# Performance work log

Measured on AMD Instinct MI355X. Metric: run time of the kernel, lower is better.

The kernel has to match this reference:

```python
import jax, jax.numpy as jnp
import numpy as np
from jax import lax

EPS = 1e-5
NUM_CLASSES = 133


def conv2d(x, w, stride, pad, b=None):
    # x: [N,C,H,W], w: [O,I,kh,kw]
    out = lax.conv_general_dilated(x, w, (stride, stride), ((pad, pad), (pad, pad)),
                                   dimension_numbers=('NCHW', 'OIHW', 'NCHW'))
    if b is not None:
        out = out + b[None, :, None, None]
    return out


def cbn(x, y, embed_w, C):
    # ConditionalBatchNorm2d in training mode: batch stats (biased var), affine from embedding
    mean = x.mean(axis=(0, 2, 3), keepdims=True)
    var = x.var(axis=(0, 2, 3), keepdims=True)
    xn = (x - mean) * lax.rsqrt(var + EPS)
    gb = embed_w[y]                      # [O, 2C]
    gamma, beta = gb[:, :C], gb[:, C:]
    return gamma[:, :, None, None] * xn + beta[:, :, None, None]


def lrelu(x):
    return jnp.where(x >= 0, x, 0.2 * x)


def clstm_layer(x_seq, w, b, hidden_dim):
    # x_seq: [T, B, Cin, 16, 16] -> (all h: [T,B,hid,16,16], last h: [B,hid,16,16])
    B = x_seq.shape[1]
    h0 = jnp.zeros((B, hidden_dim, 16, 16), x_seq.dtype)

    def step(carry, x):
        h, c = carry
        cc = conv2d(jnp.concatenate([x, h], axis=1), w, 1, 2, b)  # k=5, pad=2
        i, f, o, g = jnp.split(cc, 4, axis=1)
        c = jax.nn.sigmoid(f) * c + jax.nn.sigmoid(i) * jnp.tanh(g)
        h = jax.nn.sigmoid(o) * jnp.tanh(c)
        return (h, c), h

    (h, _), hs = lax.scan(step, (h0, h0), x_seq)
    return hs, h


def setup_inputs() -> dict:
    key = jax.random.key(0)
    ks = jax.random.split(key, 24)
    O, C_in, H = 8, 512, 254
    B, T = 4, 2
    d = {}
    d['h'] = jax.random.normal(ks[0], (O, C_in, H, H), jnp.float32)
    d['objs'] = jax.random.randint(ks[1], (O,), 0, NUM_CLASSES)
    d['obj_to_img'] = jnp.repeat(jnp.arange(B), T)  # sorted, equal-sized groups

    def w(k, shape):
        fan_in = shape[1] * shape[2] * shape[3]
        return jax.random.normal(k, shape, jnp.float32) / np.sqrt(fan_in)

    def embed(k, C):
        g = 1.0 + 0.02 * jax.random.normal(k, (NUM_CLASSES, C), jnp.float32)
        return jnp.concatenate([g, jnp.zeros((NUM_CLASSES, C), jnp.float32)], axis=1)

    d['c1_w'] = w(ks[2], (32, 512, 1, 1))
    d['c2_w'] = w(ks[3], (64, 32, 4, 4))
    d['c3_w'] = w(ks[4], (128, 64, 4, 4))
    d['c4_w'] = w(ks[5], (256, 128, 4, 4))
    d['c5_w'] = w(ks[6], (512, 256, 4, 4))
    d['e1'] = embed(ks[7], 32)
    d['e2'] = embed(ks[8], 64)
    d['e3'] = embed(ks[9], 128)
    d['e4'] = embed(ks[10], 256)
    d['e5'] = embed(ks[11], 512)
    # ConvLSTM layers: hidden [128, 64, 64], kernel 5x5, input_dim 512
    d['lw0'] = w(ks[12], (4 * 128, 512 + 128, 5, 5))
    d['lb0'] = jnp.zeros((4 * 128,), jnp.float32)
    d['lw1'] = w(ks[13], (4 * 64, 128 + 64, 5, 5))
    d['lb1'] = jnp.zeros((4 * 64,), jnp.float32)
    d['lw2'] = w(ks[14], (4 * 64, 64 + 64, 5, 5))
    d['lb2'] = jnp.zeros((4 * 64,), jnp.float32)
    return d


def reference(objs, obj_to_img, h, c1_w, c2_w, c3_w, c4_w, c5_w,
              e1, e2, e3, e4, e5, lw0, lb0, lw1, lb1, lw2, lb2):
    x = lrelu(cbn(conv2d(h, c1_w, 1, 1), objs, e1, 32))    # [O,32,256,256]
    x = lrelu(cbn(conv2d(x, c2_w, 2, 1), objs, e2, 64))    # [O,64,128,128]
    x = lrelu(cbn(conv2d(x, c3_w, 2, 1), objs, e3, 128))   # [O,128,64,64]
    x = cbn(conv2d(x, c4_w, 2, 1), objs, e4, 256)          # no activation after bn4 (as in source)
    x = cbn(conv2d(x, c5_w, 2, 1), objs, e5, 512)          # [O,512,16,16], no activation after bn5

    # Group ragged per-image object sequences. The torch loop groups consecutive
    # equal obj_to_img ids; with equal group sizes this is a static reshape.
    o2i = np.asarray(obj_to_img)
    B = int(o2i.max()) + 1
    O = x.shape[0]
    T = O // B
    assert B * T == O, 'reference assumes equal-sized, sorted object groups'
    seq = x.reshape(B, T, 512, 16, 16).transpose(1, 0, 2, 3, 4)  # [T,B,512,16,16]

    hs, _ = clstm_layer(seq, lw0, lb0, 128)
    hs, _ = clstm_layer(hs, lw1, lb1, 64)
    _, h_last = clstm_layer(hs, lw2, lb2, 64)
    return h_last  # [B,64,16,16]
```

## Files before the change

kernel.cpp:

```cpp
#include <hip/hip_runtime.h>
#include <math.h>

#define LEAK 0.2f

typedef __attribute__((ext_vector_type(8))) short bf16x8;
typedef __attribute__((ext_vector_type(4))) float f32x4;

__device__ __forceinline__ unsigned short f2bf(float f) {
  unsigned u = __float_as_uint(f);
  u += 0x7FFFu + ((u >> 16) & 1u);
  return (unsigned short)(u >> 16);
}
__device__ __forceinline__ unsigned pack2(float a, float b) {
  return (unsigned)f2bf(a) | ((unsigned)f2bf(b) << 16);
}

#define MFMA16(a, b, c) __builtin_amdgcn_mfma_f32_16x16x32_bf16(a, b, c, 0, 0, 0)

__device__ __forceinline__ void wprep_std(
    const float* __restrict__ w, unsigned short* __restrict__ dst,
    int O, int C, int TAPS, int i)
{
  int o = i / (C * TAPS);
  int r = i - o * C * TAPS;
  int c = r / TAPS, tap = r - c * TAPS;
  dst[((size_t)tap * O + o) * C + c] = f2bf(w[i]);
}

__global__ __launch_bounds__(256) void wprepAll_kernel(
    const float* c1w, const float* c2w, const float* c3w, const float* c4w,
    const float* c5w, const float* lw0, const float* lw1, const float* lw2,
    unsigned short* wb1, unsigned short* wb2, unsigned short* wb3,
    unsigned short* wb4, unsigned short* wb5, unsigned short* wbf0,
    unsigned short* wbf1, unsigned short* wbf2)
{
  int i = blockIdx.x * 256 + threadIdx.x;
  if (i < 16384) {
    int o = i >> 9, c = i & 511;
    wb1[(((c >> 5) * 32) + o) * 32 + (c & 31)] = f2bf(c1w[i]);
    return;
  }
  i -= 16384;
  if (i < 32768)   { wprep_std(c2w, wb2, 64, 32, 16, i);    return; }
  i -= 32768;
  if (i < 131072)  { wprep_std(c3w, wb3, 128, 64, 16, i);   return; }
  i -= 131072;
  if (i < 524288)  { wprep_std(c4w, wb4, 256, 128, 16, i);  return; }
  i -= 524288;
  if (i < 2097152) { wprep_std(c5w, wb5, 512, 256, 16, i);  return; }
  i -= 2097152;
  if (i < 8192000) { wprep_std(lw0, wbf0, 512, 640, 25, i); return; }
  i -= 8192000;
  if (i < 1228800) { wprep_std(lw1, wbf1, 256, 192, 25, i); return; }
  i -= 1228800;
  if (i < 819200)  { wprep_std(lw2, wbf2, 256, 128, 25, i); return; }
}

__global__ __launch_bounds__(256) void conv1M_kernel(
    const float* __restrict__ h, const unsigned short* __restrict__ wbc,
    float* __restrict__ xT, float* __restrict__ part1)
{
  __shared__ __align__(16) unsigned short inT[2][256 * 40];
  __shared__ float red1[4][4][2][4][2];

  const int n = blockIdx.y, r = blockIdx.x;
  const int px0 = r * 256;
  const int tid = threadIdx.x, lane = tid & 63, wid = tid >> 6;
  const int ln15 = lane & 15, kg = lane >> 4;
  const bool rint = (r >= 1 && r <= 254);

  f32x4 acc[2][4];
#pragma unroll
  for (int m = 0; m < 2; ++m)
#pragma unroll
    for (int f = 0; f < 4; ++f) acc[m][f] = (f32x4){0.f, 0.f, 0.f, 0.f};

#define STAGE1(KC, BUF)                                                          \
  {                                                                              \
    _Pragma("unroll")                                                            \
    for (int k = 0; k < 4; ++k) {                                                \
      const int ch = 2 * (k * 4 + wid);                                          \
      const int c0 = 4 * lane;                                                   \
      const float* p0 = h + ((size_t)(n * 512 + (KC) * 32 + ch)) * 64516         \
                          + (size_t)(r - 1) * 254 + (c0 - 1);                    \
      const float* p1 = p0 + 64516;                                              \
      float v0[4], v1[4];                                                        \
      _Pragma("unroll")                                                          \
      for (int j = 0; j < 4; ++j) {                                              \
        const int c = c0 + j;                                                    \
        const bool ok = rint && (c >= 1) && (c <= 254);                          \
        v0[j] = ok ? p0[j] : 0.f;                                                \
        v1[j] = ok ? p1[j] : 0.f;                                                \
      }                                                                          \
      const int chs = ch ^ ((lane & 3) << 3);                                    \
      _Pragma("unroll")                                                          \
      for (int j = 0; j < 4; ++j)                                                \
        *(unsigned*)&inT[BUF][(c0 + j) * 40 + chs] = pack2(v0[j], v1[j]);        \
    }                                                                            \
  }

  STAGE1(0, 0);
  __syncthreads();
  for (int kc = 0; kc < 16; ++kc) {
    if (kc < 15) STAGE1(kc + 1, (kc + 1) & 1);
    const bf16x8 a0 = *(const bf16x8*)(wbc + ((size_t)(kc * 32 + ln15)) * 32 + kg * 8);
    const bf16x8 a1 = *(const bf16x8*)(wbc + ((size_t)(kc * 32 + 16 + ln15)) * 32 + kg * 8);
    const int cur = kc & 1;
#pragma unroll
    for (int f = 0; f < 4; ++f) {
      const int pxr = wid * 64 + f * 16 + ln15;
      const int chs = (kg * 8) ^ (((pxr >> 2) & 3) << 3);
      const bf16x8 b = *(const bf16x8*)&inT[cur][pxr * 40 + chs];
      acc[0][f] = MFMA16(a0, b, acc[0][f]);
      acc[1][f] = MFMA16(a1, b, acc[1][f]);
    }
    __syncthreads();
  }
#undef STAGE1

#pragma unroll
  for (int mf = 0; mf < 2; ++mf) {
#pragma unroll
    for (int f = 0; f < 4; ++f) {
      const int px = px0 + wid * 64 + f * 16 + ln15;
      const int o = mf * 16 + kg * 4;
      *(f32x4*)(xT + ((size_t)n * 65536 + px) * 32 + o) = acc[mf][f];
    }
  }

#pragma unroll
  for (int mf = 0; mf < 2; ++mf) {
#pragma unroll
    for (int j = 0; j < 4; ++j) {
      float s = 0.f, q = 0.f;
#pragma unroll
      for (int f = 0; f < 4; ++f) { float v = acc[mf][f][j]; s += v; q += v * v; }
#pragma unroll
      for (int mk = 1; mk < 16; mk <<= 1) {
        s += __shfl_xor(s, mk);
        q += __shfl_xor(q, mk);
      }
      if (ln15 == 0) { red1[wid][kg][mf][j][0] = s; red1[wid][kg][mf][j][1] = q; }
    }
  }
  __syncthreads();
  if (tid < 32) {
    const int mf = tid >> 4, kgi = (tid >> 2) & 3, j = tid & 3;
    float s = red1[0][kgi][mf][j][0] + red1[1][kgi][mf][j][0]
            + red1[2][kgi][mf][j][0] + red1[3][kgi][mf][j][0];
    float q = red1[0][kgi][mf][j][1] + red1[1][kgi][mf][j][1]
            + red1[2][kgi][mf][j][1] + red1[3][kgi][mf][j][1];
    atomicAdd(&part1[tid], s);
    atomicAdd(&part1[32 + tid], q);
  }
}

__global__ __launch_bounds__(256) void cbn1T_kernel(
    const float* __restrict__ xT, const float* __restrict__ part1, float invN,
    const float* __restrict__ e1, const int* __restrict__ objs,
    unsigned short* __restrict__ T2)
{
  __shared__ float st[32][4];
  const int n = blockIdx.y;
  if (threadIdx.x < 32) {
    int y = objs[n];
    float s = part1[threadIdx.x], q = part1[32 + threadIdx.x];
    float mean = s * invN;
    st[threadIdx.x][0] = mean;
    st[threadIdx.x][1] = rsqrtf(q * invN - mean * mean + 1e-5f);
    st[threadIdx.x][2] = e1[(size_t)y * 64 + threadIdx.x];
    st[threadIdx.x][3] = e1[(size_t)y * 64 + 32 + threadIdx.x];
  }
  __syncthreads();
  const int pix = blockIdx.x * 256 + threadIdx.x;
  const int r = pix >> 8, c = pix & 255;
  const float* src = xT + ((size_t)n * 65536 + pix) * 32;
  unsigned short* dst = T2 + ((size_t)n * 66564 + (size_t)(r + 1) * 258 + (c + 1)) * 32;
  unsigned outw[16];
#pragma unroll
  for (int q = 0; q < 8; ++q) {
    float4 t = ((const float4*)src)[q];
    float v[4] = {t.x, t.y, t.z, t.w};
#pragma unroll
    for (int j = 0; j < 4; ++j) {
      int ch = q * 4 + j;
      float z = (v[j] - st[ch][0]) * st[ch][1] * st[ch][2] + st[ch][3];
      v[j] = z >= 0.f ? z : LEAK * z;
    }
    outw[2 * q]     = pack2(v[0], v[1]);
    outw[2 * q + 1] = pack2(v[2], v[3]);
  }
  uint4* d4 = (uint4*)dst;
#pragma unroll
  for (int q = 0; q < 4; ++q)
    d4[q] = make_uint4(outw[4*q], outw[4*q+1], outw[4*q+2], outw[4*q+3]);
}

template <int C, int O, int H, int WM>
__global__ __launch_bounds__(256) void conv4T_kernel(
    const unsigned short* __restrict__ Tin, const unsigned short* __restrict__ wb,
    float* __restrict__ raw, float* __restrict__ part)
{
  constexpr int HIN2 = 2 * H + 2;
  constexpr int KC = C / 32;
  constexpr int WN4 = 4 / WM;
  constexpr int NT = WM;
  constexpr int LOGH = (H == 128 ? 7 : (H == 64 ? 6 : (H == 32 ? 5 : 4)));
  __shared__ float red[4][4][2][4][2];
  const int o0 = blockIdx.x * (WM * 32);
  const int strip = blockIdx.y;
  const int n = blockIdx.z;
  const int tid = threadIdx.x, lane = tid & 63, wid = tid >> 6;
  const int wm = wid / WN4, wn = wid % WN4;
  const int ln15 = lane & 15, kg = lane >> 4;
  const unsigned short* inb = Tin + (size_t)n * (HIN2 * HIN2) * C;

  f32x4 acc[2][NT];
#pragma unroll
  for (int m = 0; m < 2; ++m)
#pragma unroll
    for (int nt = 0; nt < NT; ++nt) acc[m][nt] = (f32x4){0.f, 0.f, 0.f, 0.f};

  int r_[NT], c_[NT];
#pragma unroll
  for (int nt = 0; nt < NT; ++nt) {
    const int gp = strip * 64 + (wn * NT + nt) * 16;
    r_[nt] = gp >> LOGH;
    c_[nt] = (gp & (H - 1)) + ln15;
  }

  for (int kc = 0; kc < KC; ++kc) {
    const int cb = kc * 32 + kg * 8;
#pragma unroll
    for (int tap = 0; tap < 16; ++tap) {
      const int ky = tap >> 2, kx = tap & 3;
      const unsigned short* ap = wb + ((size_t)tap * O + o0 + wm * 32 + ln15) * C + cb;
      bf16x8 a0 = *(const bf16x8*)ap;
      bf16x8 a1 = *(const bf16x8*)(ap + (size_t)16 * C);
#pragma unroll
      for (int nt = 0; nt < NT; ++nt) {
        bf16x8 b = *(const bf16x8*)(inb + (size_t)((2 * r_[nt] + ky) * HIN2 + 2 * c_[nt] + kx) * C + cb);
        acc[0][nt] = MFMA16(a0, b, acc[0][nt]);
        acc[1][nt] = MFMA16(a1, b, acc[1][nt]);
      }
    }
  }

#pragma unroll
  for (int mf = 0; mf < 2; ++mf) {
    const int o = o0 + wm * 32 + mf * 16 + kg * 4;
#pragma unroll
    for (int nt = 0; nt < NT; ++nt) {
      const int gp = strip * 64 + (wn * NT + nt) * 16 + ln15;
      *(f32x4*)(raw + ((size_t)n * (H * H) + gp) * O + o) = acc[mf][nt];
    }
  }

#pragma unroll
  for (int mf = 0; mf < 2; ++mf) {
#pragma unroll
    for (int j = 0; j < 4; ++j) {
      float s = 0.f, q = 0.f;
#pragma unroll
      for (int nt = 0; nt < NT; ++nt) { float v = acc[mf][nt][j]; s += v; q += v * v; }
#pragma unroll
      for (int mk = 1; mk < 16; mk <<= 1) {
        s += __shfl_xor(s, mk);
        q += __shfl_xor(q, mk);
      }
      if (ln15 == 0) { red[wid][kg][mf][j][0] = s; red[wid][kg][mf][j][1] = q; }
    }
  }
  __syncthreads();
  if (tid < WM * 32) {
    const int wmi = tid >> 5, mf = (tid >> 4) & 1, kgi = (tid >> 2) & 3, j = tid & 3;
    float s = 0.f, q = 0.f;
#pragma unroll
    for (int w = 0; w < WN4; ++w) {
      s += red[wmi * WN4 + w][kgi][mf][j][0];
      q += red[wmi * WN4 + w][kgi][mf][j][1];
    }
    atomicAdd(&part[o0 + tid], s);
    atomicAdd(&part[O + o0 + tid], q);
  }
}

template <int C, int H, int P2, int CSO, bool LRELU, bool LMAP>
__global__ __launch_bounds__(256) void cbnT_kernel(
    const float* __restrict__ raw, const float* __restrict__ part, float invN,
    const float* __restrict__ embed, const int* __restrict__ objs,
    unsigned short* __restrict__ Tout)
{
  constexpr int W2 = H + 2 * P2;
  constexpr int LOGH = (H == 128 ? 7 : (H == 64 ? 6 : (H == 32 ? 5 : 4)));
  const int n = blockIdx.y;
  const int y = objs[n];
  const int pix = blockIdx.x * 64 + (threadIdx.x >> 2);
  const int r = pix >> LOGH, c = pix & (H - 1);
  const float* src = raw + ((size_t)n * (H * H) + pix) * C;
  const size_t nb = LMAP ? (size_t)((n & 1) * 4 + (n >> 1)) * (W2 * W2) * CSO
                         : (size_t)n * (W2 * W2) * CSO;
  unsigned short* dst = Tout + nb + ((size_t)(r + P2) * W2 + c + P2) * CSO;
  const float* gam = embed + (size_t)y * 2 * C;
  const float* bet = gam + C;
  for (int cs = (threadIdx.x & 3); cs < C / 8; cs += 4) {
    float4 ps0 = ((const float4*)part)[cs * 2],       ps1 = ((const float4*)part)[cs * 2 + 1];
    float4 pq0 = ((const float4*)(part + C))[cs * 2], pq1 = ((const float4*)(part + C))[cs * 2 + 1];
    float4 g0 = ((const float4*)gam)[cs * 2], g1 = ((const float4*)gam)[cs * 2 + 1];
    float4 b0 = ((const float4*)bet)[cs * 2], b1 = ((const float4*)bet)[cs * 2 + 1];
    float4 v0 = ((const float4*)src)[cs * 2], v1 = ((const float4*)src)[cs * 2 + 1];
    float sv[8] = {ps0.x, ps0.y, ps0.z, ps0.w, ps1.x, ps1.y, ps1.z, ps1.w};
    float qv[8] = {pq0.x, pq0.y, pq0.z, pq0.w, pq1.x, pq1.y, pq1.z, pq1.w};
    float gv[8] = {g0.x, g0.y, g0.z, g0.w, g1.x, g1.y, g1.z, g1.w};
    float bv[8] = {b0.x, b0.y, b0.z, b0.w, b1.x, b1.y, b1.z, b1.w};
    float vv[8] = {v0.x, v0.y, v0.z, v0.w, v1.x, v1.y, v1.z, v1.w};
    float o_[8];
#pragma unroll
    for (int k = 0; k < 8; ++k) {
      float m = sv[k] * invN;
      float rs = rsqrtf(qv[k] * invN - m * m + 1e-5f);
      float z = (vv[k] - m) * rs * gv[k] + bv[k];
      o_[k] = (LRELU && z < 0.f) ? LEAK * z : z;
    }
    ((uint4*)dst)[cs] = make_uint4(pack2(o_[0], o_[1]), pack2(o_[2], o_[3]),
                                   pack2(o_[4], o_[5]), pack2(o_[6], o_[7]));
  }
}

template <int O, int CS, int WM, int WN>
__global__ __launch_bounds__(256) void conv5L_kernel(
    const unsigned short* __restrict__ Lin, const unsigned short* __restrict__ wbf,
    float* __restrict__ pp, int kbeg, int slot0, size_t lin_tstr, size_t pp_tstr)
{
  constexpr int FN = 16 / WN;
  const int o0 = blockIdx.x * (WM * 32);
  const int b = blockIdx.y & 3, t = blockIdx.y >> 2;
  const int ks = blockIdx.z;
  const int tid = threadIdx.x, lane = tid & 63, wid = tid >> 6;
  const int wm = wid / WN, wn = wid % WN;
  const int ln15 = lane & 15, kg = lane >> 4;
  const unsigned short* inb = Lin + (size_t)t * lin_tstr + (size_t)b * 400 * CS;
  float* ppb = pp + (size_t)t * pp_tstr + ((size_t)(slot0 + ks) * 4 + b) * (256 * O);

  f32x4 acc[2][FN];
#pragma unroll
  for (int m = 0; m < 2; ++m)
#pragma unroll
    for (int nt = 0; nt < FN; ++nt) acc[m][nt] = (f32x4){0.f, 0.f, 0.f, 0.f};

  const int cb = (kbeg + ks) * 32 + kg * 8;
  for (int tap = 0; tap < 25; ++tap) {
    const int ty = tap / 5, tx = tap - 5 * ty;
    const unsigned short* ap = wbf + ((size_t)tap * O + o0 + wm * 32 + ln15) * CS + cb;
    bf16x8 a0 = *(const bf16x8*)ap;
    bf16x8 a1 = *(const bf16x8*)(ap + (size_t)16 * CS);
#pragma unroll
    for (int nt = 0; nt < FN; ++nt) {
      const int p = (wn * FN + nt) * 16 + ln15;
      const int prow = p >> 4, pcol = p & 15;
      bf16x8 bfv = *(const bf16x8*)(inb + (size_t)((prow + ty) * 20 + pcol + tx) * CS + cb);
      acc[0][nt] = MFMA16(a0, bfv, acc[0][nt]);
      acc[1][nt] = MFMA16(a1, bfv, acc[1][nt]);
    }
  }

#pragma unroll
  for (int mf = 0; mf < 2; ++mf) {
    const int o = o0 + wm * 32 + mf * 16 + kg * 4;
#pragma unroll
    for (int nt = 0; nt < FN; ++nt) {
      const int pix = (wn * FN + nt) * 16 + ln15;
      *(f32x4*)(ppb + (size_t)pix * O + o) = acc[mf][nt];
    }
  }
}

template <int Hc, int CS, int CX, int CSN>
__global__ __launch_bounds__(256) void lstm_pointT_kernel(
    const float* __restrict__ pp, int KS, const float* __restrict__ bias,
    float* __restrict__ cT, unsigned short* __restrict__ own,
    unsigned short* __restrict__ nxt, float* __restrict__ fout)
{
  constexpr int C4 = Hc / 4;
  constexpr int O = 4 * Hc;
  constexpr int LOGC4 = (C4 == 32 ? 5 : 4);
  const int i = blockIdx.x * 256 + threadIdx.x;
  const int c4 = i & (C4 - 1);
  const int pix = (i >> LOGC4) & 255;
  const int b = i >> (LOGC4 + 8);

  float g[4][4];
#pragma unroll
  for (int gt = 0; gt < 4; ++gt)
#pragma unroll
    for (int j = 0; j < 4; ++j) g[gt][j] = 0.f;

  for (int ks = 0; ks < KS; ++ks) {
    const float* base = pp + (((size_t)(ks * 4 + b)) * 256 + pix) * O + c4 * 4;
#pragma unroll
    for (int gt = 0; gt < 4; ++gt) {
      float4 v = *(const float4*)(base + gt * Hc);
      g[gt][0] += v.x; g[gt][1] += v.y; g[gt][2] += v.z; g[gt][3] += v.w;
    }
  }
#pragma unroll
  for (int gt = 0; gt < 4; ++gt) {
    float4 bv = *(const float4*)(bias + gt * Hc + c4 * 4);
    g[gt][0] += bv.x; g[gt][1] += bv.y; g[gt][2] += bv.z; g[gt][3] += bv.w;
  }

  float* cp = cT + ((size_t)b * 256 + pix) * Hc + c4 * 4;
  float4 cold = *(const float4*)cp;
  float co[4] = {cold.x, cold.y, cold.z, cold.w};
  float hn[4];
#pragma unroll
  for (int j = 0; j < 4; ++j) {
    float si = 1.f / (1.f + expf(-g[0][j]));
    float sf = 1.f / (1.f + expf(-g[1][j]));
    float so = 1.f / (1.f + expf(-g[2][j]));
    float cn = sf * co[j] + si * tanhf(g[3][j]);
    co[j] = cn;
    hn[j] = so * tanhf(cn);
  }
  *(float4*)cp = make_float4(co[0], co[1], co[2], co[3]);

  const int prow = pix >> 4, pcol = pix & 15;
  const int ppix = (prow + 2) * 20 + pcol + 2;
  uint2 hb = make_uint2(pack2(hn[0], hn[1]), pack2(hn[2], hn[3]));
  if (own) *(uint2*)(own + ((size_t)b * 400 + ppix) * CS + CX + c4 * 4) = hb;
  if (nxt) *(uint2*)(nxt + ((size_t)b * 400 + ppix) * CSN + c4 * 4) = hb;
  if (fout) {
#pragma unroll
    for (int j = 0; j < 4; ++j)
      fout[((size_t)b * Hc + c4 * 4 + j) * 256 + pix] = hn[j];
  }
}

extern "C" void kernel_launch(void* const* d_in, const int* in_sizes, int n_in,
                              void* d_out, int out_size, void* d_ws, size_t ws_size,
                              hipStream_t stream)
{
  const float* h    = (const float*)d_in[0];
  const int*   objs = (const int*)  d_in[1];
  const float* c1w  = (const float*)d_in[3];
  const float* c2w  = (const float*)d_in[4];
  const float* c3w  = (const float*)d_in[5];
  const float* c4w  = (const float*)d_in[6];
  const float* c5w  = (const float*)d_in[7];
  const float* e1   = (const float*)d_in[8];
  const float* e2   = (const float*)d_in[9];
  const float* e3   = (const float*)d_in[10];
  const float* e4   = (const float*)d_in[11];
  const float* e5   = (const float*)d_in[12];
  const float* lw0  = (const float*)d_in[13];
  const float* lb0  = (const float*)d_in[14];
  const float* lw1  = (const float*)d_in[15];
  const float* lb1  = (const float*)d_in[16];
  const float* lw2  = (const float*)d_in[17];
  const float* lb2  = (const float*)d_in[18];

  char* p = (char*)d_ws;
  auto alloc = [&](size_t bytes) { char* r = p; p += (bytes + 255) & ~(size_t)255; return r; };
  float* x1T  = (float*)alloc((size_t)8 * 65536 * 32 * 4);
  float* raw2 = (float*)alloc((size_t)8 * 16384 * 64 * 4);
  float* raw3 = (float*)alloc((size_t)8 * 4096 * 128 * 4);
  float* raw4 = (float*)alloc((size_t)8 * 1024 * 256 * 4);
  float* raw5 = (float*)alloc((size_t)8 * 256 * 512 * 4);
  float* pp   = (float*)alloc((size_t)2 * 20 * 4 * 256 * 512 * 4);
  unsigned short* wb1  = (unsigned short*)alloc((size_t)32 * 512 * 2);
  unsigned short* wb2  = (unsigned short*)alloc((size_t)16 * 64 * 32 * 2);
  unsigned short* wb3  = (unsigned short*)alloc((size_t)16 * 128 * 64 * 2);
  unsigned short* wb4  = (unsigned short*)alloc((size_t)16 * 256 * 128 * 2);
  unsigned short* wb5  = (unsigned short*)alloc((size_t)16 * 512 * 256 * 2);
  unsigned short* wbf0 = (unsigned short*)alloc((size_t)25 * 512 * 640 * 2);
  unsigned short* wbf1 = (unsigned short*)alloc((size_t)25 * 256 * 192 * 2);
  unsigned short* wbf2 = (unsigned short*)alloc((size_t)25 * 256 * 128 * 2);
  char* zbase = p;
  unsigned short* T2 = (unsigned short*)alloc((size_t)8 * 66564 * 32 * 2);
  unsigned short* T3 = (unsigned short*)alloc((size_t)8 * 16900 * 64 * 2);
  unsigned short* T4 = (unsigned short*)alloc((size_t)8 * 4356 * 128 * 2);
  unsigned short* T5 = (unsigned short*)alloc((size_t)8 * 1156 * 256 * 2);
  unsigned short* L0in = (unsigned short*)alloc((size_t)2 * 4 * 400 * 640 * 2);
  unsigned short* L1in = (unsigned short*)alloc((size_t)2 * 4 * 400 * 192 * 2);
  unsigned short* L2in = (unsigned short*)alloc((size_t)2 * 4 * 400 * 128 * 2);
  float* cT0 = (float*)alloc((size_t)4 * 256 * 128 * 4);
  float* cT1 = (float*)alloc((size_t)4 * 256 * 64 * 4);
  float* cT2 = (float*)alloc((size_t)4 * 256 * 64 * 4);
  float* part1 = (float*)alloc(2 * 32 * 4);
  float* part2 = (float*)alloc(2 * 64 * 4);
  float* part3 = (float*)alloc(2 * 128 * 4);
  float* part4 = (float*)alloc(2 * 256 * 4);
  float* part5 = (float*)alloc(2 * 512 * 4);
  size_t zsize = (size_t)(p - zbase);

  hipMemsetAsync(zbase, 0, zsize, stream);
  wprepAll_kernel<<<(13041664 + 255) / 256, 256, 0, stream>>>(
      c1w, c2w, c3w, c4w, c5w, lw0, lw1, lw2,
      wb1, wb2, wb3, wb4, wb5, wbf0, wbf1, wbf2);

  conv1M_kernel<<<dim3(256, 8), 256, 0, stream>>>(h, wb1, x1T, part1);
  cbn1T_kernel<<<dim3(256, 8), 256, 0, stream>>>(x1T, part1, 1.f / (float)(8 * 65536), e1, objs, T2);

  conv4T_kernel<32, 64, 128, 2><<<dim3(1, 256, 8), 256, 0, stream>>>(T2, wb2, raw2, part2);
  cbnT_kernel<64, 128, 1, 64, true, false><<<dim3(256, 8), 256, 0, stream>>>(
      raw2, part2, 1.f / (float)(8 * 16384), e2, objs, T3);

  conv4T_kernel<64, 128, 64, 2><<<dim3(2, 64, 8), 256, 0, stream>>>(T3, wb3, raw3, part3);
  cbnT_kernel<128, 64, 1, 128, true, false><<<dim3(64, 8), 256, 0, stream>>>(
      raw3, part3, 1.f / (float)(8 * 4096), e3, objs, T4);

  conv4T_kernel<128, 256, 32, 1><<<dim3(8, 16, 8), 256, 0, stream>>>(T4, wb4, raw4, part4);
  cbnT_kernel<256, 32, 1, 256, false, false><<<dim3(16, 8), 256, 0, stream>>>(
      raw4, part4, 1.f / (float)(8 * 1024), e4, objs, T5);

  conv4T_kernel<256, 512, 16, 1><<<dim3(16, 4, 8), 256, 0, stream>>>(T5, wb5, raw5, part5);
  cbnT_kernel<512, 16, 2, 640, false, true><<<dim3(4, 8), 256, 0, stream>>>(
      raw5, part5, 1.f / (float)(8 * 256), e5, objs, L0in);

  {
    const size_t LINT = (size_t)4 * 400 * 640;
    const size_t PPT  = (size_t)20 * 4 * 256 * 512;
    conv5L_kernel<512, 640, 2, 2><<<dim3(8, 8, 16), 256, 0, stream>>>(
        L0in, wbf0, pp, 0, 0, LINT, PPT);
    lstm_pointT_kernel<128, 640, 512, 192><<<128, 256, 0, stream>>>(
        pp, 16, lb0, cT0, L0in + LINT, L1in, nullptr);
    conv5L_kernel<512, 640, 2, 2><<<dim3(8, 4, 4), 256, 0, stream>>>(
        L0in + LINT, wbf0, pp + PPT, 16, 16, 0, 0);
    lstm_pointT_kernel<128, 640, 512, 192><<<128, 256, 0, stream>>>(
        pp + PPT, 20, lb0, cT0, nullptr, L1in + (size_t)4 * 400 * 192, nullptr);
  }

  {
    const size_t LINT = (size_t)4 * 400 * 192;
    const size_t PPT  = (size_t)6 * 4 * 256 * 256;
    conv5L_kernel<256, 192, 1, 4><<<dim3(8, 8, 4), 256, 0, stream>>>(
        L1in, wbf1, pp, 0, 0, LINT, PPT);
    lstm_pointT_kernel<64, 192, 128, 128><<<64, 256, 0, stream>>>(
        pp, 4, lb1, cT1, L1in + LINT, L2in, nullptr);
    conv5L_kernel<256, 192, 1, 4><<<dim3(8, 4, 2), 256, 0, stream>>>(
        L1in + LINT, wbf1, pp + PPT, 4, 4, 0, 0);
    lstm_pointT_kernel<64, 192, 128, 128><<<64, 256, 0, stream>>>(
        pp + PPT, 6, lb1, cT1, nullptr, L2in + (size_t)4 * 400 * 128, nullptr);
  }

  {
    const size_t LINT = (size_t)4 * 400 * 128;
    const size_t PPT  = (size_t)4 * 4 * 256 * 256;
    conv5L_kernel<256, 128, 1, 4><<<dim3(8, 8, 2), 256, 0, stream>>>(
        L2in, wbf2, pp, 0, 0, LINT, PPT);
    lstm_pointT_kernel<64, 128, 64, 1><<<64, 256, 0, stream>>>(
        pp, 2, lb2, cT2, L2in + LINT, nullptr, nullptr);
    conv5L_kernel<256, 128, 1, 4><<<dim3(8, 4, 2), 256, 0, stream>>>(
        L2in + LINT, wbf2, pp + PPT, 2, 2, 0, 0);
    lstm_pointT_kernel<64, 128, 64, 1><<<64, 256, 0, stream>>>(
        pp + PPT, 4, lb2, cT2, nullptr, nullptr, (float*)d_out);
  }
}
```

Baseline: 1.095 ms.

## Transpose weight prep through LDS and widen conv1 tile to two rows

Weight conversion is restructured so each block loads contiguous (o,c,tap) data into shared memory and writes each tap plane with coalesced stores, replacing scattered per-element writes. The first 1x1 conv now processes 512 pixels per block with more accumulators per wave. It drops double-buffered staging in favor of a simple load-sync-compute loop. This trades load/compute overlap for larger tiles and fewer blocks.

Result: faster. 1.041 ms (-4.9%).

```diff
diff --git a/kernel.cpp b/kernel.cpp
--- a/kernel.cpp
+++ b/kernel.cpp
@@ -17,112 +17,110 @@
 
 #define MFMA16(a, b, c) __builtin_amdgcn_mfma_f32_16x16x32_bf16(a, b, c, 0, 0, 0)
 
-__device__ __forceinline__ void wprep_std(
-    const float* __restrict__ w, unsigned short* __restrict__ dst,
-    int O, int C, int TAPS, int i)
-{
-  int o = i / (C * TAPS);
-  int r = i - o * C * TAPS;
-  int c = r / TAPS, tap = r - c * TAPS;
-  dst[((size_t)tap * O + o) * C + c] = f2bf(w[i]);
-}
-
-__global__ __launch_bounds__(256) void wprepAll_kernel(
+__global__ __launch_bounds__(256) void wprepT_kernel(
     const float* c1w, const float* c2w, const float* c3w, const float* c4w,
     const float* c5w, const float* lw0, const float* lw1, const float* lw2,
     unsigned short* wb1, unsigned short* wb2, unsigned short* wb3,
     unsigned short* wb4, unsigned short* wb5, unsigned short* wbf0,
     unsigned short* wbf1, unsigned short* wbf2)
 {
-  int i = blockIdx.x * 256 + threadIdx.x;
-  if (i < 16384) {
+  __shared__ float lds[256 * 26];
+  const int tid = threadIdx.x;
+  int b = blockIdx.x;
+
+  const float* src;
+  unsigned short* dst;
+  int T, OC, base;
+  if (b < 8)         { src = c2w; dst = wb2;  T = 16; OC = 2048;   base = b * 256; }
+  else if (b < 40)   { src = c3w; dst = wb3;  T = 16; OC = 8192;   base = (b - 8) * 256; }
+  else if (b < 168)  { src = c4w; dst = wb4;  T = 16; OC = 32768;  base = (b - 40) * 256; }
+  else if (b < 680)  { src = c5w; dst = wb5;  T = 16; OC = 131072; base = (b - 168) * 256; }
+  else if (b < 872)  { src = lw1; dst = wbf1; T = 25; OC = 49152;  base = (b - 680) * 256; }
+  else if (b < 1000) { src = lw2; dst = wbf2; T = 25; OC = 32768;  base = (b - 872) * 256; }
+  else if (b < 2280) { src = lw0; dst = wbf0; T = 25; OC = 327680; base = (b - 1000) * 256; }
+  else {
+    int i = (b - 2280) * 256 + tid;
     int o = i >> 9, c = i & 511;
     wb1[(((c >> 5) * 32) + o) * 32 + (c & 31)] = f2bf(c1w[i]);
     return;
   }
-  i -= 16384;
-  if (i < 32768)   { wprep_std(c2w, wb2, 64, 32, 16, i);    return; }
-  i -= 32768;
-  if (i < 131072)  { wprep_std(c3w, wb3, 128, 64, 16, i);   return; }
-  i -= 131072;
-  if (i < 524288)  { wprep_std(c4w, wb4, 256, 128, 16, i);  return; }
-  i -= 524288;
-  if (i < 2097152) { wprep_std(c5w, wb5, 512, 256, 16, i);  return; }
-  i -= 2097152;
-  if (i < 8192000) { wprep_std(lw0, wbf0, 512, 640, 25, i); return; }
-  i -= 8192000;
-  if (i < 1228800) { wprep_std(lw1, wbf1, 256, 192, 25, i); return; }
-  i -= 1228800;
-  if (i < 819200)  { wprep_std(lw2, wbf2, 256, 128, 25, i); return; }
+
+  const float* sp = src + (size_t)base * T;
+  for (int e = tid; e < 256 * T; e += 256) {
+    int oc = e / T, tap = e - oc * T;
+    lds[oc * 26 + tap] = sp[e];
+  }
+  __syncthreads();
+  for (int tap = 0; tap < T; ++tap)
+    dst[(size_t)tap * OC + base + tid] = f2bf(lds[tid * 26 + tap]);
 }
 
 __global__ __launch_bounds__(256) void conv1M_kernel(
     const float* __restrict__ h, const unsigned short* __restrict__ wbc,
     float* __restrict__ xT, float* __restrict__ part1)
 {
-  __shared__ __align__(16) unsigned short inT[2][256 * 40];
+  __shared__ __align__(16) unsigned short inT[512 * 40];
   __shared__ float red1[4][4][2][4][2];
 
-  const int n = blockIdx.y, r = blockIdx.x;
-  const int px0 = r * 256;
+  const int n = blockIdx.y;
+  const int px0 = blockIdx.x * 512;
   const int tid = threadIdx.x, lane = tid & 63, wid = tid >> 6;
   const int ln15 = lane & 15, kg = lane >> 4;
-  const bool rint = (r >= 1 && r <= 254);
-
-  f32x4 acc[2][4];
+
+  f32x4 acc[2][8];
 #pragma unroll
   for (int m = 0; m < 2; ++m)
 #pragma unroll
-    for (int f = 0; f < 4; ++f) acc[m][f] = (f32x4){0.f, 0.f, 0.f, 0.f};
-
-#define STAGE1(KC, BUF)                                                          \
-  {                                                                              \
-    _Pragma("unroll")                                                            \
-    for (int k = 0; k < 4; ++k) {                                                \
-      const int ch = 2 * (k * 4 + wid);                                          \
-      const int c0 = 4 * lane;                                                   \
-      const float* p0 = h + ((size_t)(n * 512 + (KC) * 32 + ch)) * 64516         \
-                          + (size_t)(r - 1) * 254 + (c0 - 1);                    \
-      const float* p1 = p0 + 64516;                                              \
-      float v0[4], v1[4];                                                        \
-      _Pragma("unroll")                                                          \
-      for (int j = 0; j < 4; ++j) {                                              \
-        const int c = c0 + j;                                                    \
-        const bool ok = rint && (c >= 1) && (c <= 254);                          \
-        v0[j] = ok ? p0[j] : 0.f;                                                \
-        v1[j] = ok ? p1[j] : 0.f;                                                \
-      }                                                                          \
-      const int chs = ch ^ ((lane & 3) << 3);                                    \
-      _Pragma("unroll")                                                          \
-      for (int j = 0; j < 4; ++j)                                                \
-        *(unsigned*)&inT[BUF][(c0 + j) * 40 + chs] = pack2(v0[j], v1[j]);        \
-    }                                                                            \
-  }
-
-  STAGE1(0, 0);
-  __syncthreads();
+    for (int f = 0; f < 8; ++f) acc[m][f] = (f32x4){0.f, 0.f, 0.f, 0.f};
+
   for (int kc = 0; kc < 16; ++kc) {
-    if (kc < 15) STAGE1(kc + 1, (kc + 1) & 1);
+    __syncthreads();
+#pragma unroll
+    for (int k = 0; k < 8; ++k) {
+      const int u = tid + k * 256;
+      const int chp = u >> 7;
+      const int pxq = u & 127;
+      const int ch = 2 * chp;
+      const int pxl = 4 * pxq;
+      const int pxg = px0 + pxl;
+      const int r = pxg >> 8;
+      const int c0 = pxg & 255;
+      const bool rint = (r >= 1 && r <= 254);
+      const float* hrow0 = h + ((size_t)(n * 512 + kc * 32 + ch)) * 64516
+                             + (size_t)(r - 1) * 254 + (c0 - 1);
+      const float* hrow1 = hrow0 + 64516;
+      float v0[4], v1[4];
+#pragma unroll
+      for (int j = 0; j < 4; ++j) {
+        const int c = c0 + j;
+        const bool ok = rint && (c >= 1) && (c <= 254);
+        v0[j] = ok ? hrow0[j] : 0.f;
+        v1[j] = ok ? hrow1[j] : 0.f;
+      }
+      const int chs = ch ^ ((pxq & 3) << 3);
+#pragma unroll
+      for (int j = 0; j < 4; ++j)
+        *(unsigned*)&inT[(pxl + j) * 40 + chs] = pack2(v0[j], v1[j]);
+    }
+    __syncthreads();
+
     const bf16x8 a0 = *(const bf16x8*)(wbc + ((size_t)(kc * 32 + ln15)) * 32 + kg * 8);
     const bf16x8 a1 = *(const bf16x8*)(wbc + ((size_t)(kc * 32 + 16 + ln15)) * 32 + kg * 8);
-    const int cur = kc & 1;
-#pragma unroll
-    for (int f = 0; f < 4; ++f) {
-      const int pxr = wid * 64 + f * 16 + ln15;
+#pragma unroll
+    for (int f = 0; f < 8; ++f) {
+      const int pxr = wid * 128 + f * 16 + ln15;
       const int chs = (kg * 8) ^ (((pxr >> 2) & 3) << 3);
-      const bf16x8 b = *(const bf16x8*)&inT[cur][pxr * 40 + chs];
+      const bf16x8 b = *(const bf16x8*)&inT[pxr * 40 + chs];
       acc[0][f] = MFMA16(a0, b, acc[0][f]);
       acc[1][f] = MFMA16(a1, b, acc[1][f]);
     }
-    __syncthreads();
-  }
-#undef STAGE1
+  }
 
 #pragma unroll
   for (int mf = 0; mf < 2; ++mf) {
 #pragma unroll
-    for (int f = 0; f < 4; ++f) {
-      const int px = px0 + wid * 64 + f * 16 + ln15;
+    for (int f = 0; f < 8; ++f) {
+      const int px = px0 + wid * 128 + f * 16 + ln15;
       const int o = mf * 16 + kg * 4;
       *(f32x4*)(xT + ((size_t)n * 65536 + px) * 32 + o) = acc[mf][f];
     }
@@ -134,7 +132,7 @@
     for (int j = 0; j < 4; ++j) {
       float s = 0.f, q = 0.f;
 #pragma unroll
-      for (int f = 0; f < 4; ++f) { float v = acc[mf][f][j]; s += v; q += v * v; }
+      for (int f = 0; f < 8; ++f) { float v = acc[mf][f][j]; s += v; q += v * v; }
 #pragma unroll
       for (int mk = 1; mk < 16; mk <<= 1) {
         s += __shfl_xor(s, mk);
@@ -494,11 +492,11 @@
   size_t zsize = (size_t)(p - zbase);
 
   hipMemsetAsync(zbase, 0, zsize, stream);
-  wprepAll_kernel<<<(13041664 + 255) / 256, 256, 0, stream>>>(
+  wprepT_kernel<<<2344, 256, 0, stream>>>(
       c1w, c2w, c3w, c4w, c5w, lw0, lw1, lw2,
       wb1, wb2, wb3, wb4, wb5, wbf0, wbf1, wbf2);
 
-  conv1M_kernel<<<dim3(256, 8), 256, 0, stream>>>(h, wb1, x1T, part1);
+  conv1M_kernel<<<dim3(128, 8), 256, 0, stream>>>(h, wb1, x1T, part1);
   cbn1T_kernel<<<dim3(256, 8), 256, 0, stream>>>(x1T, part1, 1.f / (float)(8 * 65536), e1, objs, T2);
 
   conv4T_kernel<32, 64, 128, 2><<<dim3(1, 256, 8), 256, 0, stream>>>(T2, wb2, raw2, part2);
```
